# Kernel tuning notes

Hardware: AMD Instinct MI355X
Metric: run time of the kernel (lower is better)

Reference implementation:

```python
import jax, jax.numpy as jnp
import numpy as np

D_MODEL = 1024
N_HEADS = 16
D_K = D_MODEL // N_HEADS


def setup_inputs() -> dict:
    key = jax.random.key(0)
    ks = jax.random.split(key, 5)
    s = 1.0 / np.sqrt(D_MODEL)
    x = jax.random.normal(ks[0], (4, 2048, D_MODEL), dtype=jnp.float32)
    W_qkv = jax.random.normal(ks[1], (D_MODEL, 3 * D_MODEL), dtype=jnp.float32) * s
    b_qkv = jnp.zeros((3 * D_MODEL,), dtype=jnp.float32)
    W_proj = jax.random.normal(ks[2], (D_MODEL, D_MODEL), dtype=jnp.float32) * s
    b_proj = jnp.zeros((D_MODEL,), dtype=jnp.float32)
    return {"x": x, "W_qkv": W_qkv, "b_qkv": b_qkv, "W_proj": W_proj, "b_proj": b_proj}


def reference(x, W_qkv, b_qkv, W_proj, b_proj):
    B, T, C = x.shape
    qkv = x @ W_qkv + b_qkv  # [B,T,3C]
    q, k, v = jnp.split(qkv, 3, axis=2)
    # [B,T,C] -> [B,H,T,dk]
    def to_heads(t):
        return t.reshape(B, T, N_HEADS, D_K).transpose(0, 2, 1, 3)
    q, k, v = to_heads(q), to_heads(k), to_heads(v)
    scale = 1.0 / np.sqrt(D_K)
    att = jnp.einsum('bhqd,bhkd->bhqk', q, k) * scale
    causal = jnp.tril(jnp.ones((T, T), dtype=bool))
    att = jnp.where(causal, att, -jnp.inf)
    att = jax.nn.softmax(att, axis=-1)
    y = jnp.einsum('bhqk,bhkd->bhqd', att, v)
    y = y.transpose(0, 2, 1, 3).reshape(B, T, C)
    return y @ W_proj + b_proj
```

## Files before the change

kernel.cpp:

```cpp
#include <hip/hip_runtime.h>
#include <stdint.h>


typedef float  floatx4 __attribute__((ext_vector_type(4)));
typedef __bf16 bf16x8  __attribute__((ext_vector_type(8)));
typedef __bf16 bf16x4  __attribute__((ext_vector_type(4)));

#define AS1 __attribute__((address_space(1)))
#define AS3 __attribute__((address_space(3)))

__device__ __forceinline__ void gload_lds16(const void* g, void* l) {
    __builtin_amdgcn_global_load_lds((AS1 void*)(uintptr_t)g,
                                     (AS3 void*)(uintptr_t)l, 16, 0, 0);
}

#if __has_builtin(__builtin_amdgcn_exp2f)
#define EXP2F(x) __builtin_amdgcn_exp2f(x)
#else
#define EXP2F(x) exp2f(x)
#endif

#define LOG2E 1.44269504088896340736f
#define ATT_SC (0.125f * LOG2E)
#define MASK_NEG (-3.0e4f)

static constexpr int Bn = 4, Tn = 2048, Cn = 1024, Hn = 16, DKn = 64;
static constexpr int BT = Bn * Tn;
static constexpr int N_QKV = 3 * Cn;
static constexpr int PAD = 68;


__global__ void cast_x_kernel(const float* __restrict__ x, __bf16* __restrict__ xb, int n) {
    int i = (blockIdx.x * blockDim.x + threadIdx.x) * 4;
    if (i < n) {
        float4 v = *(const float4*)(x + i);
        bf16x4 o;
        o[0] = (__bf16)v.x; o[1] = (__bf16)v.y; o[2] = (__bf16)v.z; o[3] = (__bf16)v.w;
        *(bf16x4*)(xb + i) = o;
    }
}

__global__ void transpose_cast_kernel(const float* __restrict__ W, __bf16* __restrict__ WT,
                                      int R, int C) {
    __shared__ float tile[32][33];
    int tx = threadIdx.x & 31, ty = threadIdx.x >> 5;
    int r0 = blockIdx.y * 32, c0 = blockIdx.x * 32;
#pragma unroll
    for (int i = 0; i < 4; i++)
        tile[ty + i * 8][tx] = W[(size_t)(r0 + ty + i * 8) * C + c0 + tx];
    __syncthreads();
#pragma unroll
    for (int i = 0; i < 4; i++)
        WT[(size_t)(c0 + ty + i * 8) * R + r0 + tx] = (__bf16)tile[tx][ty + i * 8];
}

__global__ __launch_bounds__(256) void gemm_qkv_kernel(
    const __bf16* __restrict__ A, const __bf16* __restrict__ Bt,
    const float* __restrict__ bias,
    __bf16* __restrict__ Qo, __bf16* __restrict__ Ko, __bf16* __restrict__ Vo) {
    const int K = 1024;
    __shared__ __bf16 Al[128 * 32];
    __shared__ __bf16 Bl[128 * 32];
    int tid = threadIdx.x, w = tid >> 6, lane = tid & 63;
    int lq = lane >> 4, l16 = lane & 15;
    int bm = blockIdx.y, bn = blockIdx.x;
    int wm = w & 1, wn = w >> 1;

    const __bf16* Ag = A + (size_t)(bm * 128 + w * 32 + (lane >> 2)) * K + (lane & 3) * 8;
    const __bf16* Bg = Bt + (size_t)(bn * 128 + w * 32 + (lane >> 2)) * K + (lane & 3) * 8;
    __bf16* AlW = Al + w * 32 * 32;
    __bf16* BlW = Bl + w * 32 * 32;

    floatx4 acc[4][4] = {};
    for (int k0 = 0; k0 < K; k0 += 32) {
        __syncthreads();
        gload_lds16(Ag + k0, AlW);
        gload_lds16(Ag + k0 + 16 * K, AlW + 16 * 32);
        gload_lds16(Bg + k0, BlW);
        gload_lds16(Bg + k0 + 16 * K, BlW + 16 * 32);
        __syncthreads();
        bf16x8 af[4], bf[4];
#pragma unroll
        for (int i = 0; i < 4; i++)
            af[i] = *(const bf16x8*)&Al[(wm * 64 + i * 16 + l16) * 32 + lq * 8];
#pragma unroll
        for (int i = 0; i < 4; i++)
            bf[i] = *(const bf16x8*)&Bl[(wn * 64 + i * 16 + l16) * 32 + lq * 8];
#pragma unroll
        for (int mt = 0; mt < 4; mt++)
#pragma unroll
            for (int nt = 0; nt < 4; nt++)
                acc[mt][nt] = __builtin_amdgcn_mfma_f32_16x16x32_bf16(
                    af[mt], bf[nt], acc[mt][nt], 0, 0, 0);
    }
#pragma unroll
    for (int nt = 0; nt < 4; nt++) {
        int gbase = bn * 128 + wn * 64 + nt * 16;
        int gcol = gbase + l16;
        int which = gbase >> 10;
        float bv = bias[gcol];
        if (which == 2) {
            int hh = (gbase - 2048) >> 6;
            int dd = ((gbase - 2048) & 63) + l16;
#pragma unroll
            for (int mt = 0; mt < 4; mt++) {
                int growb = bm * 128 + wm * 64 + mt * 16 + lq * 4;
                int bb = growb >> 11, tt = growb & 2047;
                bf16x4 v4;
#pragma unroll
                for (int r = 0; r < 4; r++) v4[r] = (__bf16)(acc[mt][nt][r] + bv);
                *(bf16x4*)&Vo[((size_t)(bb * 16 + hh) * 64 + dd) * 2048 + tt] = v4;
            }
        } else {
            int rem = gbase & 1023;
            int hh = rem >> 6, dd = (rem & 63) + l16;
            __bf16* dst = (which == 0) ? Qo : Ko;
            float scl = (which == 0) ? ATT_SC : 1.0f;
#pragma unroll
            for (int mt = 0; mt < 4; mt++) {
#pragma unroll
                for (int r = 0; r < 4; r++) {
                    int grow = bm * 128 + wm * 64 + mt * 16 + lq * 4 + r;
                    int bb = grow >> 11, tt = grow & 2047;
                    dst[((size_t)(bb * 16 + hh) * 2048 + tt) * 64 + dd] =
                        (__bf16)((acc[mt][nt][r] + bv) * scl);
                }
            }
        }
    }
}

__global__ __launch_bounds__(256) void gemm_proj_kernel(
    const __bf16* __restrict__ A, const __bf16* __restrict__ Bt,
    const float* __restrict__ bias, float* __restrict__ out) {
    const int K = 1024;
    __shared__ __bf16 Al[128 * 32];
    __shared__ __bf16 Bl[128 * 32];
    int tid = threadIdx.x, w = tid >> 6, lane = tid & 63;
    int lq = lane >> 4, l16 = lane & 15;
    int bm = blockIdx.y, bn = blockIdx.x;
    int wm = w & 1, wn = w >> 1;

    const __bf16* Ag = A + (size_t)(bm * 128 + w * 32 + (lane >> 2)) * K + (lane & 3) * 8;
    const __bf16* Bg = Bt + (size_t)(bn * 128 + w * 32 + (lane >> 2)) * K + (lane & 3) * 8;
    __bf16* AlW = Al + w * 32 * 32;
    __bf16* BlW = Bl + w * 32 * 32;

    floatx4 acc[4][4] = {};
    for (int k0 = 0; k0 < K; k0 += 32) {
        __syncthreads();
        gload_lds16(Ag + k0, AlW);
        gload_lds16(Ag + k0 + 16 * K, AlW + 16 * 32);
        gload_lds16(Bg + k0, BlW);
        gload_lds16(Bg + k0 + 16 * K, BlW + 16 * 32);
        __syncthreads();
        bf16x8 af[4], bf[4];
#pragma unroll
        for (int i = 0; i < 4; i++)
            af[i] = *(const bf16x8*)&Al[(wm * 64 + i * 16 + l16) * 32 + lq * 8];
#pragma unroll
        for (int i = 0; i < 4; i++)
            bf[i] = *(const bf16x8*)&Bl[(wn * 64 + i * 16 + l16) * 32 + lq * 8];
#pragma unroll
        for (int mt = 0; mt < 4; mt++)
#pragma unroll
            for (int nt = 0; nt < 4; nt++)
                acc[mt][nt] = __builtin_amdgcn_mfma_f32_16x16x32_bf16(
                    af[mt], bf[nt], acc[mt][nt], 0, 0, 0);
    }
#pragma unroll
    for (int nt = 0; nt < 4; nt++) {
        int gcol = bn * 128 + wn * 64 + nt * 16 + l16;
        float bv = bias[gcol];
#pragma unroll
        for (int mt = 0; mt < 4; mt++) {
#pragma unroll
            for (int r = 0; r < 4; r++) {
                int grow = bm * 128 + wm * 64 + mt * 16 + lq * 4 + r;
                out[(size_t)grow * 1024 + gcol] = acc[mt][nt][r] + bv;
            }
        }
    }
}

__global__ __launch_bounds__(256) void attn_kernel(
    const __bf16* __restrict__ Q, const __bf16* __restrict__ K,
    const __bf16* __restrict__ Vt, __bf16* __restrict__ Y) {
    const int bid = blockIdx.x;
    const int pr = bid >> 6, bh = bid & 63;
    const int b = bh >> 4, h = bh & 15;
    int tid = threadIdx.x, w = tid >> 6, lane = tid & 63;
    int lq = lane >> 4, l16 = lane & 15;

    const __bf16* Qh = Q + (size_t)bh * Tn * DKn;
    const __bf16* Kh = K + (size_t)bh * Tn * DKn;
    const __bf16* Vh = Vt + (size_t)bh * DKn * Tn;

    __shared__ __bf16 Kl[64 * PAD];
    __shared__ __bf16 Vl[64 * PAD];
    __shared__ __bf16 Pl[128 * PAD];

    int srow = tid >> 3, ssl = tid & 7;

    bf16x8 onesf;
#pragma unroll
    for (int j = 0; j < 8; j++) onesf[j] = (__bf16)1.0f;

    bf16x8 kr0 = *(const bf16x8*)&Kh[(size_t)srow * 64 + ssl * 8];
    bf16x8 kr1 = *(const bf16x8*)&Kh[(size_t)(srow + 32) * 64 + ssl * 8];
    bf16x8 vr0 = *(const bf16x8*)&Vh[(size_t)srow * 2048 + ssl * 8];
    bf16x8 vr1 = *(const bf16x8*)&Vh[(size_t)(srow + 32) * 2048 + ssl * 8];

#pragma unroll
    for (int seg = 0; seg < 2; seg++) {
        const int qt = seg ? (15 - pr) : pr;
        const int q0 = qt * 128;
        const int ktmax = 2 * qt + 1;

        bf16x8 qf[2][2];
#pragma unroll
        for (int mt = 0; mt < 2; mt++)
#pragma unroll
            for (int ks = 0; ks < 2; ks++)
                qf[mt][ks] = *(const bf16x8*)&Qh[(size_t)(q0 + w * 32 + mt * 16 + l16) * 64 +
                                                 ks * 32 + lq * 8];

        floatx4 oacc[2][5] = {};

        for (int kt = 0; kt <= ktmax; kt++) {
            __syncthreads();
            *(bf16x8*)&Kl[srow * PAD + ssl * 8] = kr0;
            *(bf16x8*)&Kl[(srow + 32) * PAD + ssl * 8] = kr1;
            *(bf16x8*)&Vl[srow * PAD + ssl * 8] = vr0;
            *(bf16x8*)&Vl[(srow + 32) * PAD + ssl * 8] = vr1;
            __syncthreads();
            if (!(seg == 1 && kt == ktmax)) {
                int nk = (kt < ktmax) ? (kt + 1) : 0;
                kr0 = *(const bf16x8*)&Kh[(size_t)(nk * 64 + srow) * 64 + ssl * 8];
                kr1 = *(const bf16x8*)&Kh[(size_t)(nk * 64 + srow + 32) * 64 + ssl * 8];
                vr0 = *(const bf16x8*)&Vh[(size_t)srow * 2048 + nk * 64 + ssl * 8];
                vr1 = *(const bf16x8*)&Vh[(size_t)(srow + 32) * 2048 + nk * 64 + ssl * 8];
            }

            floatx4 s2[2][4] = {};
#pragma unroll
            for (int ks = 0; ks < 2; ks++) {
                bf16x8 kf[4];
#pragma unroll
                for (int nt = 0; nt < 4; nt++)
                    kf[nt] = *(const bf16x8*)&Kl[(nt * 16 + l16) * PAD + ks * 32 + lq * 8];
#pragma unroll
                for (int mt = 0; mt < 2; mt++)
#pragma unroll
                    for (int nt = 0; nt < 4; nt++)
                        s2[mt][nt] = __builtin_amdgcn_mfma_f32_16x16x32_bf16(
                            qf[mt][ks], kf[nt], s2[mt][nt], 0, 0, 0);
            }

            if (kt >= 2 * qt) {
#pragma unroll
                for (int mt = 0; mt < 2; mt++)
#pragma unroll
                    for (int nt = 0; nt < 4; nt++) {
                        int col = kt * 64 + nt * 16 + l16;
#pragma unroll
                        for (int r = 0; r < 4; r++) {
                            int row = q0 + w * 32 + mt * 16 + lq * 4 + r;
                            if (col > row) s2[mt][nt][r] = MASK_NEG;
                        }
                    }
            }

#pragma unroll
            for (int mt = 0; mt < 2; mt++) {
#pragma unroll
                for (int nt = 0; nt < 4; nt++) {
#pragma unroll
                    for (int r = 0; r < 4; r++) {
                        float p = EXP2F(s2[mt][nt][r]);
                        int rowl = w * 32 + mt * 16 + lq * 4 + r;
                        Pl[rowl * PAD + nt * 16 + l16] = (__bf16)p;
                    }
                }
            }

#pragma unroll
            for (int ks = 0; ks < 2; ks++) {
                bf16x8 pf[2], vf[4];
#pragma unroll
                for (int mt = 0; mt < 2; mt++)
                    pf[mt] = *(const bf16x8*)&Pl[(w * 32 + mt * 16 + l16) * PAD + ks * 32 + lq * 8];
#pragma unroll
                for (int dt = 0; dt < 4; dt++)
                    vf[dt] = *(const bf16x8*)&Vl[(dt * 16 + l16) * PAD + ks * 32 + lq * 8];
#pragma unroll
                for (int mt = 0; mt < 2; mt++) {
#pragma unroll
                    for (int dt = 0; dt < 4; dt++)
                        oacc[mt][dt] = __builtin_amdgcn_mfma_f32_16x16x32_bf16(
                            pf[mt], vf[dt], oacc[mt][dt], 0, 0, 0);
                    oacc[mt][4] = __builtin_amdgcn_mfma_f32_16x16x32_bf16(
                        pf[mt], onesf, oacc[mt][4], 0, 0, 0);
                }
            }
        }

#pragma unroll
        for (int mt = 0; mt < 2; mt++) {
#pragma unroll
            for (int r = 0; r < 4; r++) {
                float inv = 1.0f / oacc[mt][4][r];
                int rowg = q0 + w * 32 + mt * 16 + lq * 4 + r;
#pragma unroll
                for (int dt = 0; dt < 4; dt++)
                    Y[((size_t)(b * 2048 + rowg)) * 1024 + h * 64 + dt * 16 + l16] =
                        (__bf16)(oacc[mt][dt][r] * inv);
            }
        }
    }
}


extern "C" void kernel_launch(void* const* d_in, const int* in_sizes, int n_in,
                              void* d_out, int out_size, void* d_ws, size_t ws_size,
                              hipStream_t stream) {
    const float* x     = (const float*)d_in[0];
    const float* Wqkv  = (const float*)d_in[1];
    const float* bqkv  = (const float*)d_in[2];
    const float* Wproj = (const float*)d_in[3];
    const float* bproj = (const float*)d_in[4];
    float* out = (float*)d_out;

    __bf16* xb     = (__bf16*)d_ws;
    __bf16* WqkvT  = xb + (size_t)BT * Cn;
    __bf16* WprojT = WqkvT + (size_t)N_QKV * Cn;
    __bf16* Qb     = WprojT + (size_t)Cn * Cn;
    __bf16* Kb     = Qb + (size_t)BT * Cn;
    __bf16* Vb     = Kb + (size_t)BT * Cn;
    __bf16* Yb     = Vb + (size_t)BT * Cn;

    int nx = BT * Cn;
    cast_x_kernel<<<(nx / 4 + 255) / 256, 256, 0, stream>>>(x, xb, nx);
    transpose_cast_kernel<<<dim3(N_QKV / 32, Cn / 32), 256, 0, stream>>>(Wqkv, WqkvT, Cn, N_QKV);
    transpose_cast_kernel<<<dim3(Cn / 32, Cn / 32), 256, 0, stream>>>(Wproj, WprojT, Cn, Cn);

    gemm_qkv_kernel<<<dim3(N_QKV / 128, BT / 128), 256, 0, stream>>>(
        xb, WqkvT, bqkv, Qb, Kb, Vb);

    attn_kernel<<<dim3(512), 256, 0, stream>>>(Qb, Kb, Vb, Yb);

    gemm_proj_kernel<<<dim3(Cn / 128, BT / 128), 256, 0, stream>>>(
        Yb, WprojT, bproj, out);
}
```

Before: 265.6 us.

## Shrink attention query tile to 64 rows and double grid size

The attention kernel now processes 64-query tiles per segment, with 16 rows per wave instead of 32, and launches 1024 blocks instead of 512. Causal pairing is kept by combining tiles pr and 31-pr, and masking is applied only on the diagonal key tile. This reduces the masked work wasted on the diagonal, raises parallelism and occupancy, and lowers register and LDS use per block. In exchange, each block reloads K/V from global memory for fewer queries, so K/V traffic doubles and each K fragment feeds half as many MFMAs.

```diff
diff --git a/kernel.cpp b/kernel.cpp
--- a/kernel.cpp
+++ b/kernel.cpp
@@ -198,7 +198,7 @@
 
     __shared__ __bf16 Kl[64 * PAD];
     __shared__ __bf16 Vl[64 * PAD];
-    __shared__ __bf16 Pl[128 * PAD];
+    __shared__ __bf16 Pl[64 * PAD];
 
     int srow = tid >> 3, ssl = tid & 7;
 
@@ -213,19 +213,17 @@
 
 #pragma unroll
     for (int seg = 0; seg < 2; seg++) {
-        const int qt = seg ? (15 - pr) : pr;
-        const int q0 = qt * 128;
-        const int ktmax = 2 * qt + 1;
-
-        bf16x8 qf[2][2];
-#pragma unroll
-        for (int mt = 0; mt < 2; mt++)
-#pragma unroll
-            for (int ks = 0; ks < 2; ks++)
-                qf[mt][ks] = *(const bf16x8*)&Qh[(size_t)(q0 + w * 32 + mt * 16 + l16) * 64 +
-                                                 ks * 32 + lq * 8];
-
-        floatx4 oacc[2][5] = {};
+        const int qt = seg ? (31 - pr) : pr;
+        const int q0 = qt * 64;
+        const int ktmax = qt;
+
+        bf16x8 qf[2];
+#pragma unroll
+        for (int ks = 0; ks < 2; ks++)
+            qf[ks] = *(const bf16x8*)&Qh[(size_t)(q0 + w * 16 + l16) * 64 +
+                                         ks * 32 + lq * 8];
+
+        floatx4 oacc[5] = {};
 
         for (int kt = 0; kt <= ktmax; kt++) {
             __syncthreads();
@@ -242,7 +240,7 @@
                 vr1 = *(const bf16x8*)&Vh[(size_t)(srow + 32) * 2048 + nk * 64 + ssl * 8];
             }
 
-            floatx4 s2[2][4] = {};
+            floatx4 s2[4] = {};
 #pragma unroll
             for (int ks = 0; ks < 2; ks++) {
                 bf16x8 kf[4];
@@ -250,72 +248,57 @@
                 for (int nt = 0; nt < 4; nt++)
                     kf[nt] = *(const bf16x8*)&Kl[(nt * 16 + l16) * PAD + ks * 32 + lq * 8];
 #pragma unroll
-                for (int mt = 0; mt < 2; mt++)
-#pragma unroll
-                    for (int nt = 0; nt < 4; nt++)
-                        s2[mt][nt] = __builtin_amdgcn_mfma_f32_16x16x32_bf16(
-                            qf[mt][ks], kf[nt], s2[mt][nt], 0, 0, 0);
-            }
-
-            if (kt >= 2 * qt) {
-#pragma unroll
-                for (int mt = 0; mt < 2; mt++)
-#pragma unroll
-                    for (int nt = 0; nt < 4; nt++) {
-                        int col = kt * 64 + nt * 16 + l16;
-#pragma unroll
-                        for (int r = 0; r < 4; r++) {
-                            int row = q0 + w * 32 + mt * 16 + lq * 4 + r;
-                            if (col > row) s2[mt][nt][r] = MASK_NEG;
-                        }
-                    }
-            }
-
-#pragma unroll
-            for (int mt = 0; mt < 2; mt++) {
+                for (int nt = 0; nt < 4; nt++)
+                    s2[nt] = __builtin_amdgcn_mfma_f32_16x16x32_bf16(
+                        qf[ks], kf[nt], s2[nt], 0, 0, 0);
+            }
+
+            if (kt == ktmax) {
 #pragma unroll
                 for (int nt = 0; nt < 4; nt++) {
+                    int col = kt * 64 + nt * 16 + l16;
 #pragma unroll
                     for (int r = 0; r < 4; r++) {
-                        float p = EXP2F(s2[mt][nt][r]);
-                        int rowl = w * 32 + mt * 16 + lq * 4 + r;
-                        Pl[rowl * PAD + nt * 16 + l16] = (__bf16)p;
+                        int row = q0 + w * 16 + lq * 4 + r;
+                        if (col > row) s2[nt][r] = MASK_NEG;
                     }
                 }
             }
 
 #pragma unroll
+            for (int nt = 0; nt < 4; nt++) {
+#pragma unroll
+                for (int r = 0; r < 4; r++) {
+                    float p = EXP2F(s2[nt][r]);
+                    int rowl = w * 16 + lq * 4 + r;
+                    Pl[rowl * PAD + nt * 16 + l16] = (__bf16)p;
+                }
+            }
+
+#pragma unroll
             for (int ks = 0; ks < 2; ks++) {
-                bf16x8 pf[2], vf[4];
-#pragma unroll
-                for (int mt = 0; mt < 2; mt++)
-                    pf[mt] = *(const bf16x8*)&Pl[(w * 32 + mt * 16 + l16) * PAD + ks * 32 + lq * 8];
+                bf16x8 pf = *(const bf16x8*)&Pl[(w * 16 + l16) * PAD + ks * 32 + lq * 8];
+                bf16x8 vf[4];
 #pragma unroll
                 for (int dt = 0; dt < 4; dt++)
                     vf[dt] = *(const bf16x8*)&Vl[(dt * 16 + l16) * PAD + ks * 32 + lq * 8];
 #pragma unroll
-                for (int mt = 0; mt < 2; mt++) {
-#pragma unroll
-                    for (int dt = 0; dt < 4; dt++)
-                        oacc[mt][dt] = __builtin_amdgcn_mfma_f32_16x16x32_bf16(
-                            pf[mt], vf[dt], oacc[mt][dt], 0, 0, 0);
-                    oacc[mt][4] = __builtin_amdgcn_mfma_f32_16x16x32_bf16(
-                        pf[mt], onesf, oacc[mt][4], 0, 0, 0);
-                }
+                for (int dt = 0; dt < 4; dt++)
+                    oacc[dt] = __builtin_amdgcn_mfma_f32_16x16x32_bf16(
+                        pf, vf[dt], oacc[dt], 0, 0, 0);
+                oacc[4] = __builtin_amdgcn_mfma_f32_16x16x32_bf16(
+                    pf, onesf, oacc[4], 0, 0, 0);
             }
         }
 
 #pragma unroll
-        for (int mt = 0; mt < 2; mt++) {
-#pragma unroll
-            for (int r = 0; r < 4; r++) {
-                float inv = 1.0f / oacc[mt][4][r];
-                int rowg = q0 + w * 32 + mt * 16 + lq * 4 + r;
-#pragma unroll
-                for (int dt = 0; dt < 4; dt++)
-                    Y[((size_t)(b * 2048 + rowg)) * 1024 + h * 64 + dt * 16 + l16] =
-                        (__bf16)(oacc[mt][dt][r] * inv);
-            }
+        for (int r = 0; r < 4; r++) {
+            float inv = 1.0f / oacc[4][r];
+            int rowg = q0 + w * 16 + lq * 4 + r;
+#pragma unroll
+            for (int dt = 0; dt < 4; dt++)
+                Y[((size_t)(b * 2048 + rowg)) * 1024 + h * 64 + dt * 16 + l16] =
+                    (__bf16)(oacc[dt][r] * inv);
         }
     }
 }
@@ -347,7 +330,7 @@
     gemm_qkv_kernel<<<dim3(N_QKV / 128, BT / 128), 256, 0, stream>>>(
         xb, WqkvT, bqkv, Qb, Kb, Vb);
 
-    attn_kernel<<<dim3(512), 256, 0, stream>>>(Qb, Kb, Vb, Yb);
+    attn_kernel<<<dim3(1024), 256, 0, stream>>>(Qb, Kb, Vb, Yb);
 
     gemm_proj_kernel<<<dim3(Cn / 128, BT / 128), 256, 0, stream>>>(
         Yb, WprojT, bproj, out);
```

Measured after the change: 269.9 us. Within noise of the previous version (+1.6%).
